# Optimization experiments

Measured on AMD Instinct MI355X. Metric: run time of the kernel, lower is better.

Reference implementation:

```python
import math
import jax, jax.numpy as jnp
import numpy as np

B, S, E, H, P = 8, 1024, 512, 8, 32
MAXD, OFFS, LW, STL, HID = 256, 8.0, 4, 4, 2048

def _lin(x, w, b):
    return x @ w.T + b

def _gelu(x):
    return jax.nn.gelu(x, approximate=False)  # torch nn.GELU default (erf)

def _ln(x, g, b, eps=1e-5):
    m = x.mean(-1, keepdims=True)
    v = ((x - m) ** 2).mean(-1, keepdims=True)
    return (x - m) / jnp.sqrt(v + eps) * g + b

def setup_inputs() -> dict:
    key = jax.random.key(0)
    ks = iter(jax.random.split(key, 40))
    def w(*shape):
        return (jax.random.normal(next(ks), shape, dtype=jnp.float32) * 0.02)
    x = jax.random.normal(next(ks), (B, S, E), dtype=jnp.float32)
    lengths = jax.random.randint(next(ks), (B,), S // 2, S + 1)
    padding_mask = jnp.arange(S)[None, :] >= lengths[:, None]  # (B,S) bool
    inp = dict(x=x, padding_mask=padding_mask)
    # local MHA (torch nn.MultiheadAttention packed in_proj)
    inp.update(in_proj_w=w(3 * E, E), in_proj_b=jnp.zeros((3 * E,), jnp.float32),
               mha_out_w=w(E, E), mha_out_b=jnp.zeros((E,), jnp.float32))
    # deformable attention projections
    for nm in ('dq', 'dk', 'dv', 'do'):
        inp[nm + '_w'] = w(E, E); inp[nm + '_b'] = jnp.zeros((E,), jnp.float32)
    inp.update(off1_w=w(E, E), off1_b=jnp.zeros((E,), jnp.float32),
               off2_w=w(H * P, E), off2_b=jnp.zeros((H * P,), jnp.float32))
    inp.update(gate1_w=w(E, 3 * E), gate1_b=jnp.zeros((E,), jnp.float32),
               gate2_w=w(E, E), gate2_b=jnp.zeros((E,), jnp.float32))
    inp.update(n1_g=jnp.ones((E,), jnp.float32), n1_b=jnp.zeros((E,), jnp.float32),
               n2_g=jnp.ones((E,), jnp.float32), n2_b=jnp.zeros((E,), jnp.float32))
    inp.update(ffn1_w=w(HID, E), ffn1_b=jnp.zeros((HID,), jnp.float32),
               ffn2_w=w(E, HID), ffn2_b=jnp.zeros((E,), jnp.float32))
    return inp

def _forward(x, padding_mask, in_proj_w, in_proj_b, mha_out_w, mha_out_b,
             dq_w, dq_b, dk_w, dk_b, dv_w, dv_b, do_w, do_b,
             off1_w, off1_b, off2_w, off2_b, gate1_w, gate1_b, gate2_w, gate2_b,
             n1_g, n1_b, n2_g, n2_b, ffn1_w, ffn1_b, ffn2_w, ffn2_b):
    Bv, Sv, Ev = x.shape
    hd = Ev // H
    pos = jnp.arange(Sv)
    # ---------------- local causal windowed MHA ----------------
    qkv = _lin(x, in_proj_w, in_proj_b)
    q, k, v = jnp.split(qkv, 3, axis=-1)
    q = q.reshape(Bv, Sv, H, hd).transpose(0, 2, 1, 3)  # bhsd
    k = k.reshape(Bv, Sv, H, hd).transpose(0, 2, 1, 3)
    v = v.reshape(Bv, Sv, H, hd).transpose(0, 2, 1, 3)
    scores = jnp.einsum('bhqd,bhkd->bhqk', q, k) / math.sqrt(hd)
    future = pos[None, :] > pos[:, None]
    too_far = (pos[:, None] - pos[None, :]) >= min(LW, STL)
    lmask = (future | too_far)[None, None] | padding_mask[:, None, None, :]
    scores = jnp.where(lmask, -jnp.inf, scores)
    allm = lmask.all(-1, keepdims=True)
    scores = jnp.where(allm, 0.0, scores)  # avoid NaN on fully-masked (padded) rows
    attn = jax.nn.softmax(scores, axis=-1)
    attn = jnp.where(lmask, 0.0, attn)
    lo = jnp.einsum('bhqk,bhkd->bhqd', attn, v).transpose(0, 2, 1, 3).reshape(Bv, Sv, Ev)
    local_out = _lin(lo, mha_out_w, mha_out_b)
    # ---------------- deformable long-history attention ----------------
    anchors = jnp.linspace(0.1, 0.9, P)
    valid_len = jnp.clip(Sv - padding_mask.sum(-1), 1, None)
    positions = pos[None, :, None].astype(jnp.float32)  # (1,S,1)
    base = anchors[None, None, :] * positions
    off = jnp.tanh(_lin(_gelu(_lin(x, off1_w, off1_b)), off2_w, off2_b))
    off = off.reshape(Bv, Sv, H, P).mean(2) * OFFS
    sampled = base + off
    sampled = jnp.clip(sampled, jnp.clip(positions - MAXD, 0, None), positions)
    sampled = jnp.minimum(sampled, (valid_len - 1).astype(jnp.float32)[:, None, None])
    sp = jnp.round(sampled).astype(jnp.int32)  # (B,S,P) sample positions
    qd = _lin(x, dq_w, dq_b)
    kd = _lin(x, dk_w, dk_b)
    vd = _lin(x, dv_w, dv_b)
    bidx = jnp.arange(Bv)[:, None, None]
    k_sp = kd[bidx, sp]  # (B,S,P,E) gathered keys
    v_sp = vd[bidx, sp]
    sc = jnp.einsum('bqd,bqpd->bqp', qd, k_sp) / math.sqrt(Ev)
    samp_inv = padding_mask[bidx, sp]
    causal_inv = sp > pos[None, :, None]
    rb = jnp.clip(pos[:, None] - (STL - 1), 0, None)
    long_mem_mask = pos[None, :] >= rb  # (S,S): forbid recent short-term positions
    extra_inv = long_mem_mask[pos[None, :, None], sp]
    inv = samp_inv | causal_inv | extra_inv
    sc = jnp.where(inv, -jnp.inf, sc)
    alli = inv.all(-1, keepdims=True)
    sc = jnp.where(alli, 0.0, sc)
    a = jax.nn.softmax(sc, axis=-1)
    a = jnp.where(inv, 0.0, a)
    long_out = _lin(jnp.einsum('bqp,bqpd->bqd', a, v_sp), do_w, do_b)
    # ---------------- gate fuse + FFN ----------------
    cat = jnp.concatenate([x, local_out, long_out], axis=-1)
    g = jax.nn.sigmoid(_lin(_gelu(_lin(cat, gate1_w, gate1_b)), gate2_w, gate2_b))
    fused = g * local_out + (1.0 - g) * long_out
    x1 = _ln(x + fused, n1_g, n1_b)
    f = _lin(_gelu(_lin(x1, ffn1_w, ffn1_b)), ffn2_w, ffn2_b)
    return _ln(x1 + f, n2_g, n2_b)

def reference(x, padding_mask, in_proj_w, in_proj_b, mha_out_w, mha_out_b,
              dq_w, dq_b, dk_w, dk_b, dv_w, dv_b, do_w, do_b,
              off1_w, off1_b, off2_w, off2_b, gate1_w, gate1_b, gate2_w, gate2_b,
              n1_g, n1_b, n2_g, n2_b, ffn1_w, ffn1_b, ffn2_w, ffn2_b):
    return _forward(x, padding_mask, in_proj_w, in_proj_b, mha_out_w, mha_out_b,
                    dq_w, dq_b, dk_w, dk_b, dv_w, dv_b, do_w, do_b,
                    off1_w, off1_b, off2_w, off2_b, gate1_w, gate1_b, gate2_w, gate2_b,
                    n1_g, n1_b, n2_g, n2_b, ffn1_w, ffn1_b, ffn2_w, ffn2_b)
```

## Files before the change

kernel.cpp:

```cpp
#include <hip/hip_runtime.h>
#include <hip/hip_bf16.h>
#include <type_traits>

typedef __hip_bfloat16 bf16;
typedef __attribute__((ext_vector_type(8))) short short8;
typedef __attribute__((ext_vector_type(4))) float floatx4;

static constexpr int kB = 8;
static constexpr int kS = 1024;
static constexpr int kE = 512;
static constexpr int kH = 8;
static constexpr int kP = 32;
static constexpr int kTok = kB * kS;
static constexpr int kHid = 2048;

__device__ __forceinline__ void load8f(const bf16* p, float* f) {
  uint4 u = *(const uint4*)p;
  const bf16* h = (const bf16*)&u;
#pragma unroll
  for (int e = 0; e < 8; e++) f[e] = __bfloat162float(h[e]);
}
__device__ __forceinline__ void store8b(bf16* p, const float* f) {
  uint4 u;
  bf16* h = (bf16*)&u;
#pragma unroll
  for (int e = 0; e < 8; e++) h[e] = __float2bfloat16(f[e]);
  *(uint4*)p = u;
}
__device__ __forceinline__ bool is_pad(const void* pm, int flag, int idx) {
  return flag ? (((const int*)pm)[idx] != 0)
              : (((const unsigned char*)pm)[idx] != 0);
}
__device__ __forceinline__ float fast_gelu(float x) {
  float u = x * (0.7978845608f + 0.044714998f * x * x);
  float e = __expf(2.0f * u);
  float t = 1.0f - 2.0f / (e + 1.0f);
  return 0.5f * x * (1.0f + t);
}
__device__ __forceinline__ void dma16(const bf16* g, bf16* l) {
  __builtin_amdgcn_global_load_lds(
      (const __attribute__((address_space(1))) unsigned int*)g,
      (__attribute__((address_space(3))) unsigned int*)l, 16, 0, 0);
}
__device__ __forceinline__ void drain_all() { __builtin_amdgcn_s_waitcnt(0); }

__global__ __launch_bounds__(256) void detect_kernel(const void* __restrict__ x,
                                                     int* __restrict__ meta) {
  __shared__ int cnt;
  if (threadIdx.x == 0) cnt = 0;
  __syncthreads();
  const unsigned short* u = (const unsigned short*)x;
  int c = 0;
  for (int i = threadIdx.x; i < 1024; i += 256) {
    int e = (u[i] >> 7) & 0xFF;
    if (e >= 0x90) c++;
  }
  if (c) atomicAdd(&cnt, c);
  __syncthreads();
  if (threadIdx.x == 0) meta[9] = (cnt > 64) ? 1 : 0;
}

__global__ __launch_bounds__(256) void meta_kernel(const void* __restrict__ pm,
                                                   int* __restrict__ meta) {
  __shared__ int bigfound;
  __shared__ int cnt[kB];
  int tid = threadIdx.x;
  if (tid == 0) bigfound = 0;
  if (tid < kB) cnt[tid] = 0;
  __syncthreads();
  const unsigned int* w = (const unsigned int*)pm;
  int f = 0;
  for (int i = tid; i < 2048; i += 256)
    if (w[i] & 0xFFFFFFFEu) f = 1;
  if (f) atomicOr(&bigfound, 1);
  __syncthreads();
  int flag = bigfound ? 0 : 1;
  for (int i = tid; i < kTok; i += 256) {
    if (is_pad(pm, flag, i)) atomicAdd(&cnt[i >> 10], 1);
  }
  __syncthreads();
  if (tid == 0) meta[0] = flag;
  if (tid < kB) {
    int vl = kS - cnt[tid];
    if (vl < 1) vl = 1;
    meta[1 + tid] = vl;
  }
}

struct CvtJob { const void* src; bf16* hi; bf16* lo; int nblk; };
struct CvtJobs { CvtJob j[13]; };
__global__ __launch_bounds__(256) void cvt_all_kernel(CvtJobs jobs,
                                                      const int* __restrict__ meta) {
  int fp = meta[9];
  int b = blockIdx.x, ji = 0;
  while (b >= jobs.j[ji].nblk) { b -= jobs.j[ji].nblk; ji++; }
  CvtJob J = jobs.j[ji];
  int i = b * 1024 + threadIdx.x * 4;
  float v[4];
  if (fp) {
    float4 f = ((const float4*)J.src)[i >> 2];
    v[0] = f.x; v[1] = f.y; v[2] = f.z; v[3] = f.w;
  } else {
    uint2 u = *(const uint2*)((const bf16*)J.src + i);
    const bf16* h = (const bf16*)&u;
#pragma unroll
    for (int e = 0; e < 4; e++) v[e] = __bfloat162float(h[e]);
  }
  uint2 uh;
  bf16* hh = (bf16*)&uh;
#pragma unroll
  for (int e = 0; e < 4; e++) hh[e] = __float2bfloat16(v[e]);
  *(uint2*)(J.hi + i) = uh;
  if (J.lo) {
    uint2 ul;
    bf16* hl = (bf16*)&ul;
#pragma unroll
    for (int e = 0; e < 4; e++)
      hl[e] = __float2bfloat16(v[e] - __bfloat162float(hh[e]));
    *(uint2*)(J.lo + i) = ul;
  }
}

struct CvtFJob { const void* src; float* dst; int n; };
struct CvtFJobs { CvtFJob j[16]; };
__global__ __launch_bounds__(256) void cvt_small_kernel(CvtFJobs jobs,
                                                        const int* __restrict__ meta) {
  int fp = meta[9];
#pragma unroll 1
  for (int ji = 0; ji < 16; ji++) {
    CvtFJob J = jobs.j[ji];
    for (int i = threadIdx.x; i < J.n; i += 256)
      J.dst[i] = fp ? ((const float*)J.src)[i]
                    : __bfloat162float(((const bf16*)J.src)[i]);
  }
}

static constexpr int BK = 32;

template <int BM, int BN, int ACT, typename OUTT>
__device__ __forceinline__ void gemm_core(const bf16* __restrict__ A,
                                          const bf16* __restrict__ W,
                                          const float* __restrict__ bias,
                                          OUTT* __restrict__ C, int N, int K,
                                          int m0, int n0) {
  constexpr int WR = (BM == 128 && BN == 128) ? 4 : 2;
  constexpr int WC = 4;
  __shared__ bf16 As[2][BM * BK];
  __shared__ bf16 Bs[2][BN * BK];
  const int tid = threadIdx.x;
  const int lane = tid & 63;
  const int wid = tid >> 6;
  int wm, wn;
  if constexpr (BM == 128 && BN == 128) {
    wm = (wid >> 1) * 64; wn = (wid & 1) * 64;
  } else {
    wm = wid * 32; wn = 0;
  }

  auto stage = [&](int buf, int kt) {
#pragma unroll
    for (int c = 0; c < BM / 64; c++) {
      int seg = c * 64 + wid * 16;
      int row = seg + (lane >> 2);
      int ch = (lane & 3) ^ ((row >> 1) & 3);
      dma16(&A[(size_t)(m0 + row) * K + kt + ch * 8], &As[buf][seg * BK]);
    }
#pragma unroll
    for (int c = 0; c < BN / 64; c++) {
      int seg = c * 64 + wid * 16;
      int row = seg + (lane >> 2);
      int ch = (lane & 3) ^ ((row >> 1) & 3);
      dma16(&W[(size_t)(n0 + row) * K + kt + ch * 8], &Bs[buf][seg * BK]);
    }
  };

  floatx4 acc[WR][WC];
#pragma unroll
  for (int i = 0; i < WR; i++)
#pragma unroll
    for (int j = 0; j < WC; j++) acc[i][j] = (floatx4)0.0f;

  stage(0, 0);
  drain_all();
  __syncthreads();
  const int niter = K / BK;
  for (int k = 0; k < niter; k++) {
    const int cur = k & 1;
    if (k + 1 < niter) stage(cur ^ 1, (k + 1) * BK);
    const int kb = lane >> 4;
    short8 af[WR], bfr[WC];
#pragma unroll
    for (int i = 0; i < WR; i++) {
      int r = wm + i * 16 + (lane & 15);
      af[i] = *(const short8*)(&As[cur][r * BK + ((kb ^ ((r >> 1) & 3)) << 3)]);
    }
#pragma unroll
    for (int j = 0; j < WC; j++) {
      int r = wn + j * 16 + (lane & 15);
      bfr[j] = *(const short8*)(&Bs[cur][r * BK + ((kb ^ ((r >> 1) & 3)) << 3)]);
    }
#pragma unroll
    for (int i = 0; i < WR; i++)
#pragma unroll
      for (int j = 0; j < WC; j++)
        acc[i][j] = __builtin_amdgcn_mfma_f32_16x16x32_bf16(bfr[j], af[i],
                                                            acc[i][j], 0, 0, 0);
    drain_all();
    __syncthreads();
  }

#pragma unroll
  for (int i = 0; i < WR; i++) {
    int row = m0 + wm + i * 16 + (lane & 15);
#pragma unroll
    for (int j = 0; j < WC; j++) {
      int col = n0 + wn + j * 16 + ((lane >> 4) << 2);
      float bv[4] = {0.f, 0.f, 0.f, 0.f};
      if (bias) {
        float4 b4 = *(const float4*)&bias[col];
        bv[0] = b4.x; bv[1] = b4.y; bv[2] = b4.z; bv[3] = b4.w;
      }
      float v[4];
#pragma unroll
      for (int r = 0; r < 4; r++) {
        v[r] = acc[i][j][r] + bv[r];
        if (ACT == 1) v[r] = fast_gelu(v[r]);
        else if (ACT == 2) v[r] = 1.0f / (1.0f + __expf(-v[r]));
      }
      size_t idx = (size_t)row * N + col;
      if constexpr (std::is_same<OUTT, float>::value) {
        *(float4*)&C[idx] = make_float4(v[0], v[1], v[2], v[3]);
      } else {
        uint2 u;
        bf16* h = (bf16*)&u;
#pragma unroll
        for (int r = 0; r < 4; r++) h[r] = __float2bfloat16(v[r]);
        *(uint2*)&C[idx] = u;
      }
    }
  }
}

template <int BM, int BN, int ACT, typename OUTT>
__global__ __launch_bounds__(256) void gemm_bt(
    const bf16* __restrict__ A, const bf16* __restrict__ W,
    const float* __restrict__ bias, OUTT* __restrict__ C, int N, int K) {
  gemm_core<BM, BN, ACT, OUTT>(A, W, bias, C, N, K, blockIdx.x * BM,
                               blockIdx.y * BN);
}

__global__ __launch_bounds__(256) void gemm_pair(
    const bf16* __restrict__ A0, const bf16* __restrict__ W0,
    const float* __restrict__ b0, bf16* __restrict__ C0,
    const bf16* __restrict__ A1, const bf16* __restrict__ W1,
    const float* __restrict__ b1, bf16* __restrict__ C1, int N, int K) {
  int nb = N >> 6;
  bool s = (int)blockIdx.y >= nb;
  gemm_core<128, 64, 0, bf16>(s ? A1 : A0, s ? W1 : W0, s ? b1 : b0,
                              s ? C1 : C0, N, K, blockIdx.x * 128,
                              (s ? (int)blockIdx.y - nb : (int)blockIdx.y) * 64);
}

__global__ __launch_bounds__(256) void gemm_gate1(
    const bf16* __restrict__ x, const bf16* __restrict__ lo,
    const bf16* __restrict__ lg, const bf16* __restrict__ W,
    const float* __restrict__ bias, bf16* __restrict__ C) {
  constexpr int BM = 128, BN = 64, WR = 2, WC = 4;
  constexpr int N = 512, K = 1536;
  __shared__ bf16 As[2][BM * BK];
  __shared__ bf16 Bs[2][BN * BK];
  const int tid = threadIdx.x;
  const int lane = tid & 63;
  const int wid = tid >> 6;
  const int wm = wid * 32, wn = 0;
  const int m0 = blockIdx.x * BM, n0 = blockIdx.y * BN;

  auto stage = [&](int buf, int kt) {
    const bf16* src = (kt < 512) ? x : (kt < 1024) ? lo : lg;
    int kk = kt & 511;
#pragma unroll
    for (int c = 0; c < 2; c++) {
      int seg = c * 64 + wid * 16;
      int row = seg + (lane >> 2);
      int ch = (lane & 3) ^ ((row >> 1) & 3);
      dma16(&src[(size_t)(m0 + row) * 512 + kk + ch * 8], &As[buf][seg * BK]);
    }
    {
      int seg = wid * 16;
      int row = seg + (lane >> 2);
      int ch = (lane & 3) ^ ((row >> 1) & 3);
      dma16(&W[(size_t)(n0 + row) * K + kt + ch * 8], &Bs[buf][seg * BK]);
    }
  };

  floatx4 acc[WR][WC];
#pragma unroll
  for (int i = 0; i < WR; i++)
#pragma unroll
    for (int j = 0; j < WC; j++) acc[i][j] = (floatx4)0.0f;

  stage(0, 0);
  drain_all();
  __syncthreads();
  const int niter = K / BK;
  for (int k = 0; k < niter; k++) {
    const int cur = k & 1;
    if (k + 1 < niter) stage(cur ^ 1, (k + 1) * BK);
    const int kb = lane >> 4;
    short8 af[WR], bfr[WC];
#pragma unroll
    for (int i = 0; i < WR; i++) {
      int r = wm + i * 16 + (lane & 15);
      af[i] = *(const short8*)(&As[cur][r * BK + ((kb ^ ((r >> 1) & 3)) << 3)]);
    }
#pragma unroll
    for (int j = 0; j < WC; j++) {
      int r = wn + j * 16 + (lane & 15);
      bfr[j] = *(const short8*)(&Bs[cur][r * BK + ((kb ^ ((r >> 1) & 3)) << 3)]);
    }
#pragma unroll
    for (int i = 0; i < WR; i++)
#pragma unroll
      for (int j = 0; j < WC; j++)
        acc[i][j] = __builtin_amdgcn_mfma_f32_16x16x32_bf16(bfr[j], af[i],
                                                            acc[i][j], 0, 0, 0);
    drain_all();
    __syncthreads();
  }

#pragma unroll
  for (int i = 0; i < WR; i++) {
    int row = m0 + wm + i * 16 + (lane & 15);
#pragma unroll
    for (int j = 0; j < WC; j++) {
      int col = n0 + wn + j * 16 + ((lane >> 4) << 2);
      float4 b4 = *(const float4*)&bias[col];
      float bv[4] = {b4.x, b4.y, b4.z, b4.w};
      uint2 u;
      bf16* h = (bf16*)&u;
#pragma unroll
      for (int r = 0; r < 4; r++)
        h[r] = __float2bfloat16(fast_gelu(acc[i][j][r] + bv[r]));
      *(uint2*)&C[(size_t)row * N + col] = u;
    }
  }
}

template <int BM, int BN, bool SPLIT, bool ALWAYS_AL>
__global__ __launch_bounds__(256) void gemm3_bt(
    const bf16* __restrict__ Ah, const bf16* __restrict__ Al,
    const bf16* __restrict__ Wh, const bf16* __restrict__ Wl,
    const float* __restrict__ bias, const int* __restrict__ meta,
    float* __restrict__ Cf, bf16* __restrict__ Chi, bf16* __restrict__ Clo,
    int N, int K) {
  constexpr int WR = 2;
  constexpr int WC = (BM == 128) ? 4 : 2;
  __shared__ bf16 Ash[BM * BK];
  __shared__ bf16 Asl[BM * BK];
  __shared__ bf16 Bsh[BN * BK];
  __shared__ bf16 Bsl[BN * BK];
  const int fp = meta[9];
  const bool use_al = fp || ALWAYS_AL;
  const int tid = threadIdx.x;
  const int lane = tid & 63;
  const int wid = tid >> 6;
  int wm, wn;
  if constexpr (BM == 128) {
    wm = wid * 32; wn = 0;
  } else {
    wm = (wid >> 1) * 32; wn = (wid & 1) * 32;
  }
  const int m0 = blockIdx.x * BM, n0 = blockIdx.y * BN;

  floatx4 acc[WR][WC];
#pragma unroll
  for (int i = 0; i < WR; i++)
#pragma unroll
    for (int j = 0; j < WC; j++) acc[i][j] = (floatx4)0.0f;

  for (int kt = 0; kt < K; kt += BK) {
#pragma unroll
    for (int c = 0; c < BM / 64; c++) {
      int seg = c * 64 + wid * 16;
      int row = seg + (lane >> 2);
      int ch = (lane & 3) ^ ((row >> 1) & 3);
      size_t g = (size_t)(m0 + row) * K + kt + ch * 8;
      dma16(&Ah[g], &Ash[seg * BK]);
      if (use_al) dma16(&Al[g], &Asl[seg * BK]);
    }
#pragma unroll
    for (int c = 0; c < BN / 64; c++) {
      int seg = c * 64 + wid * 16;
      int row = seg + (lane >> 2);
      int ch = (lane & 3) ^ ((row >> 1) & 3);
      size_t g = (size_t)(n0 + row) * K + kt + ch * 8;
      dma16(&Wh[g], &Bsh[seg * BK]);
      if (fp) dma16(&Wl[g], &Bsl[seg * BK]);
    }
    drain_all();
    __syncthreads();
    const int kb = lane >> 4;
    short8 ah[WR], al[WR], bh[WC], bl[WC];
#pragma unroll
    for (int i = 0; i < WR; i++) {
      int r = wm + i * 16 + (lane & 15);
      int ro = r * BK + ((kb ^ ((r >> 1) & 3)) << 3);
      ah[i] = *(const short8*)(&Ash[ro]);
      if (use_al) al[i] = *(const short8*)(&Asl[ro]);
    }
#pragma unroll
    for (int j = 0; j < WC; j++) {
      int r = wn + j * 16 + (lane & 15);
      int ro = r * BK + ((kb ^ ((r >> 1) & 3)) << 3);
      bh[j] = *(const short8*)(&Bsh[ro]);
      if (fp) bl[j] = *(const short8*)(&Bsl[ro]);
    }
#pragma unroll
    for (int i = 0; i < WR; i++)
#pragma unroll
      for (int j = 0; j < WC; j++) {
        acc[i][j] = __builtin_amdgcn_mfma_f32_16x16x32_bf16(bh[j], ah[i],
                                                            acc[i][j], 0, 0, 0);
        if (fp)
          acc[i][j] = __builtin_amdgcn_mfma_f32_16x16x32_bf16(
              bl[j], ah[i], acc[i][j], 0, 0, 0);
        if (use_al)
          acc[i][j] = __builtin_amdgcn_mfma_f32_16x16x32_bf16(
              bh[j], al[i], acc[i][j], 0, 0, 0);
      }
    __syncthreads();
  }

#pragma unroll
  for (int i = 0; i < WR; i++) {
    int row = m0 + wm + i * 16 + (lane & 15);
#pragma unroll
    for (int j = 0; j < WC; j++) {
      int col = n0 + wn + j * 16 + ((lane >> 4) << 2);
      float4 b4 = *(const float4*)&bias[col];
      float bv[4] = {b4.x, b4.y, b4.z, b4.w};
      if constexpr (SPLIT) {
        uint2 uh, ul;
        bf16* hh = (bf16*)&uh;
        bf16* hl = (bf16*)&ul;
#pragma unroll
        for (int r = 0; r < 4; r++) {
          float v = acc[i][j][r] + bv[r];
          float g = 0.5f * v * (1.0f + erff(v * 0.70710678118654752f));
          bf16 hi = __float2bfloat16(g);
          hh[r] = hi;
          hl[r] = __float2bfloat16(g - __bfloat162float(hi));
        }
        *(uint2*)&Chi[(size_t)row * N + col] = uh;
        *(uint2*)&Clo[(size_t)row * N + col] = ul;
      } else {
        *(float4*)&Cf[(size_t)row * N + col] =
            make_float4(acc[i][j][0] + bv[0], acc[i][j][1] + bv[1],
                        acc[i][j][2] + bv[2], acc[i][j][3] + bv[3]);
      }
    }
  }
}

__global__ __launch_bounds__(256) void local_attn_kernel(
    const bf16* __restrict__ qkv, const void* __restrict__ pm,
    const int* __restrict__ meta, bf16* __restrict__ lo) {
  int lane = threadIdx.x & 63;
  int t = blockIdx.x * 4 + (threadIdx.x >> 6);
  int b = t >> 10, s = t & 1023;
  int h = lane >> 3, sub = lane & 7;
  int flag = meta[0];
  float q[8];
  load8f(qkv + (size_t)t * 3072 + h * 64 + sub * 8, q);
  float sc[4];
  bool val[4];
#pragma unroll
  for (int w = 0; w < 4; w++) {
    int kp = s - 3 + w;
    bool v = (kp >= 0) && !is_pad(pm, flag, b * kS + kp);
    float d = 0.0f;
    if (v) {
      float kk[8];
      load8f(qkv + (size_t)(b * kS + kp) * 3072 + 512 + h * 64 + sub * 8, kk);
#pragma unroll
      for (int e = 0; e < 8; e++) d += q[e] * kk[e];
    }
    d += __shfl_xor(d, 1);
    d += __shfl_xor(d, 2);
    d += __shfl_xor(d, 4);
    sc[w] = v ? d / 8.0f : -INFINITY;
    val[w] = v;
  }
  float mx = fmaxf(fmaxf(sc[0], sc[1]), fmaxf(sc[2], sc[3]));
  float a[4] = {0.f, 0.f, 0.f, 0.f};
  if (mx != -INFINITY) {
    float ssum = 0.f;
#pragma unroll
    for (int w = 0; w < 4; w++) {
      float e = val[w] ? expf(sc[w] - mx) : 0.0f;
      a[w] = e;
      ssum += e;
    }
#pragma unroll
    for (int w = 0; w < 4; w++) a[w] /= ssum;
  }
  float o[8] = {0.f, 0.f, 0.f, 0.f, 0.f, 0.f, 0.f, 0.f};
#pragma unroll
  for (int w = 0; w < 4; w++) {
    if (val[w] && a[w] > 0.0f) {
      int kp = s - 3 + w;
      float vv[8];
      load8f(qkv + (size_t)(b * kS + kp) * 3072 + 1024 + h * 64 + sub * 8, vv);
#pragma unroll
      for (int e = 0; e < 8; e++) o[e] += a[w] * vv[e];
    }
  }
  store8b(lo + (size_t)t * kE + lane * 8, o);
}

__global__ __launch_bounds__(256) void sampler_kernel(
    const float* __restrict__ rawf, const void* __restrict__ pm,
    const int* __restrict__ meta, int* __restrict__ sp,
    unsigned int* __restrict__ invm) {
  int t = blockIdx.x * 8 + (threadIdx.x >> 5);
  int p = threadIdx.x & 31;
  int b = t >> 10, s = t & 1023;
  int flag = meta[0];
  float off = 0.0f;
#pragma unroll
  for (int h = 0; h < kH; h++) off += tanhf(rawf[(size_t)t * 256 + h * kP + p]);
  double anchor = 0.1 + 0.8 * (double)p / 31.0;
  double sampled = anchor * (double)s + (double)off;
  double lov = fmax(0.0, (double)s - 256.0);
  sampled = fmin(fmax(sampled, lov), (double)s);
  int vlen = meta[1 + b];
  sampled = fmin(sampled, (double)(vlen - 1));
  int spv = (int)rint(sampled);
  bool inv = is_pad(pm, flag, b * kS + spv) || (spv > s) ||
             (spv >= max(0, s - 3));
  sp[(size_t)t * kP + p] = spv;
  unsigned long long m = __ballot(inv);
  int lane = threadIdx.x & 63;
  if (lane == 0) invm[t] = (unsigned int)m;
  if (lane == 32) invm[t] = (unsigned int)(m >> 32);
}

__global__ __launch_bounds__(256) void long_attn_kernel(
    const bf16* __restrict__ qkv, const int* __restrict__ sp,
    const unsigned int* __restrict__ invm, bf16* __restrict__ ctx) {
  int lane = threadIdx.x & 63;
  int bid = blockIdx.x;
  int sbid = (bid & 7) * 256 + (bid >> 3);
  int t = sbid * 4 + (threadIdx.x >> 6);
  int b = t >> 10;
  int p = lane & 31;
  int row_abs = b * kS + sp[(size_t)t * kP + p];
  float q[8];
  load8f(qkv + (size_t)t * 3072 + 1536 + lane * 8, q);
  float sc_mine = 0.0f;
#pragma unroll 4
  for (int pp = 0; pp < 32; pp++) {
    int row = __shfl(row_abs, pp);
    float kk[8];
    load8f(qkv + (size_t)row * 3072 + 2048 + lane * 8, kk);
    float d = 0.0f;
#pragma unroll
    for (int e = 0; e < 8; e++) d += q[e] * kk[e];
#pragma unroll
    for (int m = 1; m < 64; m <<= 1) d += __shfl_xor(d, m);
    if (p == pp) sc_mine = d;
  }
  bool inv = (invm[t] >> p) & 1u;
  float sc = inv ? -INFINITY : sc_mine / 22.627416997969522f;
  float mx = sc;
#pragma unroll
  for (int m = 1; m < 32; m <<= 1) mx = fmaxf(mx, __shfl_xor(mx, m));
  float e = (inv || mx == -INFINITY) ? 0.0f : expf(sc - mx);
  float ssum = e;
#pragma unroll
  for (int m = 1; m < 32; m <<= 1) ssum += __shfl_xor(ssum, m);
  float a = (ssum > 0.0f) ? e / ssum : 0.0f;
  float o[8] = {0.f, 0.f, 0.f, 0.f, 0.f, 0.f, 0.f, 0.f};
#pragma unroll 4
  for (int pp = 0; pp < 32; pp++) {
    float ap = __shfl(a, pp);
    int row = __shfl(row_abs, pp);
    if (ap != 0.0f) {
      float vv[8];
      load8f(qkv + (size_t)row * 3072 + 2560 + lane * 8, vv);
#pragma unroll
      for (int e2 = 0; e2 < 8; e2++) o[e2] += ap * vv[e2];
    }
  }
  store8b(ctx + (size_t)t * kE + lane * 8, o);
}

__global__ __launch_bounds__(256) void ln1_kernel(
    const void* __restrict__ xin, const int* __restrict__ meta,
    const bf16* __restrict__ lo, const bf16* __restrict__ lg,
    const bf16* __restrict__ g, const float* __restrict__ gamma,
    const float* __restrict__ beta, bf16* __restrict__ x1b,
    float* __restrict__ x1f) {
  int lane = threadIdx.x & 63;
  int t = blockIdx.x * 4 + (threadIdx.x >> 6);
  size_t base = (size_t)t * kE + lane * 8;
  float xv[8], lov[8], lgv[8], gv[8], h[8];
  if (meta[9]) {
    const float4* xf = (const float4*)((const float*)xin + base);
    float4 a = xf[0], b2 = xf[1];
    xv[0] = a.x; xv[1] = a.y; xv[2] = a.z; xv[3] = a.w;
    xv[4] = b2.x; xv[5] = b2.y; xv[6] = b2.z; xv[7] = b2.w;
  } else {
    load8f((const bf16*)xin + base, xv);
  }
  load8f(lo + base, lov);
  load8f(lg + base, lgv);
  load8f(g + base, gv);
  float s1 = 0.f, s2 = 0.f;
#pragma unroll
  for (int e = 0; e < 8; e++) {
    h[e] = xv[e] + gv[e] * lov[e] + (1.0f - gv[e]) * lgv[e];
    s1 += h[e];
    s2 += h[e] * h[e];
  }
#pragma unroll
  for (int m = 1; m < 64; m <<= 1) {
    s1 += __shfl_xor(s1, m);
    s2 += __shfl_xor(s2, m);
  }
  float mean = s1 * (1.0f / kE);
  float var = s2 * (1.0f / kE) - mean * mean;
  float rstd = 1.0f / sqrtf(var + 1e-5f);
  float y[8];
#pragma unroll
  for (int e = 0; e < 8; e++)
    y[e] = (h[e] - mean) * rstd * gamma[lane * 8 + e] + beta[lane * 8 + e];
  store8b(x1b + base, y);
#pragma unroll
  for (int e = 0; e < 8; e++) x1f[base + e] = y[e];
}

__global__ __launch_bounds__(256) void ln2_kernel(
    const float* __restrict__ x1f, const float* __restrict__ ff,
    const float* __restrict__ gamma, const float* __restrict__ beta,
    const int* __restrict__ meta, void* __restrict__ out) {
  int lane = threadIdx.x & 63;
  int t = blockIdx.x * 4 + (threadIdx.x >> 6);
  size_t base = (size_t)t * kE + lane * 8;
  float h[8];
  float s1 = 0.f, s2 = 0.f;
#pragma unroll
  for (int e = 0; e < 8; e++) {
    h[e] = x1f[base + e] + ff[base + e];
    s1 += h[e];
    s2 += h[e] * h[e];
  }
#pragma unroll
  for (int m = 1; m < 64; m <<= 1) {
    s1 += __shfl_xor(s1, m);
    s2 += __shfl_xor(s2, m);
  }
  float mean = s1 * (1.0f / kE);
  float var = s2 * (1.0f / kE) - mean * mean;
  float rstd = 1.0f / sqrtf(var + 1e-5f);
  float y[8];
#pragma unroll
  for (int e = 0; e < 8; e++)
    y[e] = (h[e] - mean) * rstd * gamma[lane * 8 + e] + beta[lane * 8 + e];
  if (meta[9]) {
    float* of = (float*)out + base;
    ((float4*)of)[0] = make_float4(y[0], y[1], y[2], y[3]);
    ((float4*)of)[1] = make_float4(y[4], y[5], y[6], y[7]);
  } else {
    store8b((bf16*)out + base, y);
  }
}

extern "C" void kernel_launch(void* const* d_in, const int* in_sizes, int n_in,
                              void* d_out, int out_size, void* d_ws,
                              size_t ws_size, hipStream_t stream) {
  const void* x = d_in[0];
  const void* pm = d_in[1];

  char* w = (char*)d_ws;
  auto alloc = [&](size_t bytes) {
    char* p = w;
    w += (bytes + 255) & ~(size_t)255;
    return p;
  };
  bf16* qkv_all = (bf16*)alloc((size_t)kTok * 3072 * 2);
  bf16* lo_ctx = (bf16*)alloc((size_t)kTok * kE * 2);
  bf16* ctx2 = (bf16*)alloc((size_t)kTok * kE * 2);
  bf16* local_out = (bf16*)alloc((size_t)kTok * kE * 2);
  bf16* long_out = (bf16*)alloc((size_t)kTok * kE * 2);
  bf16* hbuf = (bf16*)alloc((size_t)kTok * kE * 2);
  bf16* gbuf = (bf16*)alloc((size_t)kTok * kE * 2);
  bf16* x1b = (bf16*)alloc((size_t)kTok * kE * 2);
  float* x1f = (float*)alloc((size_t)kTok * kE * 4);
  float* rawf = (float*)alloc((size_t)kTok * 256 * 4);
  int* sp = (int*)alloc((size_t)kTok * kP * 4);
  unsigned int* invm = (unsigned int*)alloc((size_t)kTok * 4);
  int* meta = (int*)alloc(256);
  bf16* x_hi = (bf16*)alloc((size_t)kTok * kE * 2);
  bf16* x_lo = (bf16*)alloc((size_t)kTok * kE * 2);
  bf16* wall = (bf16*)alloc((size_t)3072 * 512 * 2);
  bf16* mow = (bf16*)alloc(512 * 512 * 2);
  bf16* dow = (bf16*)alloc(512 * 512 * 2);
  bf16* o1h = (bf16*)alloc(512 * 512 * 2);
  bf16* o1l = (bf16*)alloc(512 * 512 * 2);
  bf16* o2h = (bf16*)alloc(256 * 512 * 2);
  bf16* o2l = (bf16*)alloc(256 * 512 * 2);
  bf16* g1w = (bf16*)alloc(512 * 1536 * 2);
  bf16* g2w = (bf16*)alloc(512 * 512 * 2);
  bf16* f1w = (bf16*)alloc((size_t)2048 * 512 * 2);
  bf16* f2w = (bf16*)alloc((size_t)512 * 2048 * 2);
  float* ball = (float*)alloc(3072 * 4);
  float* mob = (float*)alloc(512 * 4);
  float* dob = (float*)alloc(512 * 4);
  float* o1b = (float*)alloc(512 * 4);
  float* o2b = (float*)alloc(256 * 4);
  float* g1b = (float*)alloc(512 * 4);
  float* g2b = (float*)alloc(512 * 4);
  float* n1g = (float*)alloc(512 * 4);
  float* n1bt = (float*)alloc(512 * 4);
  float* n2g = (float*)alloc(512 * 4);
  float* n2bt = (float*)alloc(512 * 4);
  float* f1b = (float*)alloc(2048 * 4);
  float* f2b = (float*)alloc(512 * 4);

  bf16* h_hi = hbuf;
  bf16* h_lo = x1b;
  float* f_f32 = (float*)qkv_all;
  bf16* ffn_h = (bf16*)((char*)qkv_all + (size_t)kTok * kE * 4);

  dim3 blk(256);
  detect_kernel<<<1, blk, 0, stream>>>(x, meta);
  meta_kernel<<<1, blk, 0, stream>>>(pm, meta);

  CvtJobs J;
  auto job = [](const void* s, bf16* hi, bf16* lo, int n) {
    CvtJob j; j.src = s; j.hi = hi; j.lo = lo; j.nblk = n >> 10; return j;
  };
  J.j[0] = job(d_in[0], x_hi, x_lo, kTok * kE);
  J.j[1] = job(d_in[2], wall, nullptr, 1536 * 512);
  J.j[2] = job(d_in[6], wall + (size_t)1536 * 512, nullptr, 512 * 512);
  J.j[3] = job(d_in[8], wall + (size_t)2048 * 512, nullptr, 512 * 512);
  J.j[4] = job(d_in[10], wall + (size_t)2560 * 512, nullptr, 512 * 512);
  J.j[5] = job(d_in[4], mow, nullptr, 512 * 512);
  J.j[6] = job(d_in[12], dow, nullptr, 512 * 512);
  J.j[7] = job(d_in[14], o1h, o1l, 512 * 512);
  J.j[8] = job(d_in[16], o2h, o2l, 256 * 512);
  J.j[9] = job(d_in[18], g1w, nullptr, 512 * 1536);
  J.j[10] = job(d_in[20], g2w, nullptr, 512 * 512);
  J.j[11] = job(d_in[26], f1w, nullptr, 2048 * 512);
  J.j[12] = job(d_in[28], f2w, nullptr, 512 * 2048);
  int totblk = 0;
  for (int i = 0; i < 13; i++) totblk += J.j[i].nblk;
  cvt_all_kernel<<<totblk, blk, 0, stream>>>(J, meta);

  CvtFJobs JF;
  auto fjob = [](const void* s, float* d, int n) {
    CvtFJob j; j.src = s; j.dst = d; j.n = n; return j;
  };
  JF.j[0] = fjob(d_in[3], ball, 1536);
  JF.j[1] = fjob(d_in[7], ball + 1536, 512);
  JF.j[2] = fjob(d_in[9], ball + 2048, 512);
  JF.j[3] = fjob(d_in[11], ball + 2560, 512);
  JF.j[4] = fjob(d_in[5], mob, 512);
  JF.j[5] = fjob(d_in[13], dob, 512);
  JF.j[6] = fjob(d_in[15], o1b, 512);
  JF.j[7] = fjob(d_in[17], o2b, 256);
  JF.j[8] = fjob(d_in[19], g1b, 512);
  JF.j[9] = fjob(d_in[21], g2b, 512);
  JF.j[10] = fjob(d_in[22], n1g, 512);
  JF.j[11] = fjob(d_in[23], n1bt, 512);
  JF.j[12] = fjob(d_in[24], n2g, 512);
  JF.j[13] = fjob(d_in[25], n2bt, 512);
  JF.j[14] = fjob(d_in[27], f1b, 2048);
  JF.j[15] = fjob(d_in[29], f2b, 512);
  cvt_small_kernel<<<1, blk, 0, stream>>>(JF, meta);

  gemm_bt<128, 128, 0, bf16><<<dim3(64, 24), blk, 0, stream>>>(
      x_hi, wall, ball, qkv_all, 3072, kE);
  gemm3_bt<128, 64, true, false><<<dim3(64, 8), blk, 0, stream>>>(
      x_hi, x_lo, o1h, o1l, o1b, meta, nullptr, h_hi, h_lo, kE, kE);
  local_attn_kernel<<<2048, blk, 0, stream>>>(qkv_all, pm, meta, lo_ctx);
  gemm3_bt<64, 64, false, true><<<dim3(128, 4), blk, 0, stream>>>(
      h_hi, h_lo, o2h, o2l, o2b, meta, rawf, nullptr, nullptr, 256, kE);
  sampler_kernel<<<1024, blk, 0, stream>>>(rawf, pm, meta, sp, invm);
  long_attn_kernel<<<2048, blk, 0, stream>>>(qkv_all, sp, invm, ctx2);

  gemm_pair<<<dim3(64, 16), blk, 0, stream>>>(lo_ctx, mow, mob, local_out,
                                              ctx2, dow, dob, long_out, kE, kE);

  gemm_gate1<<<dim3(64, 8), blk, 0, stream>>>(x_hi, local_out, long_out, g1w,
                                              g1b, hbuf);
  gemm_bt<128, 64, 2, bf16><<<dim3(64, 8), blk, 0, stream>>>(
      hbuf, g2w, g2b, gbuf, kE, kE);

  ln1_kernel<<<2048, blk, 0, stream>>>(x, meta, local_out, long_out, gbuf, n1g,
                                       n1bt, x1b, x1f);
  gemm_bt<128, 128, 1, bf16><<<dim3(64, 16), blk, 0, stream>>>(
      x1b, f1w, f1b, ffn_h, kHid, kE);
  gemm_bt<128, 64, 0, float><<<dim3(64, 8), blk, 0, stream>>>(
      ffn_h, f2w, f2b, f_f32, kE, kHid);
  ln2_kernel<<<2048, blk, 0, stream>>>(x1f, f_f32, n2g, n2bt, meta, d_out);
}
```

Baseline: 457.2 us.

## Merge independent kernels into combined launches and fuse sampler into long attention

Combines the detect and meta kernels into one launch and folds the small bias conversion into the big conversion kernel as an extra block. The QKV GEMM and offset-1 split GEMM now share one grid, as do the local attention and offset-2 GEMM. The sampler is folded into long attention, which drops the sp/invm intermediate buffers. The aim is to cut launch overhead and tail idle time by running independent work together. In exchange, GEMM shared memory now comes from one buffer per kernel, and a heterogeneous grid can raise per-block resource use and lower occupancy for the lighter parts.

```diff
diff --git a/kernel.cpp b/kernel.cpp
--- a/kernel.cpp
+++ b/kernel.cpp
@@ -44,44 +44,39 @@
 }
 __device__ __forceinline__ void drain_all() { __builtin_amdgcn_s_waitcnt(0); }
 
-__global__ __launch_bounds__(256) void detect_kernel(const void* __restrict__ x,
-                                                     int* __restrict__ meta) {
+__global__ __launch_bounds__(256) void detect_meta_kernel(
+    const void* __restrict__ x, const void* __restrict__ pm,
+    int* __restrict__ meta) {
   __shared__ int cnt;
-  if (threadIdx.x == 0) cnt = 0;
+  __shared__ int bigfound;
+  __shared__ int pc[kB];
+  int tid = threadIdx.x;
+  if (tid == 0) { cnt = 0; bigfound = 0; }
+  if (tid < kB) pc[tid] = 0;
   __syncthreads();
   const unsigned short* u = (const unsigned short*)x;
   int c = 0;
-  for (int i = threadIdx.x; i < 1024; i += 256) {
+  for (int i = tid; i < 1024; i += 256) {
     int e = (u[i] >> 7) & 0xFF;
     if (e >= 0x90) c++;
   }
   if (c) atomicAdd(&cnt, c);
-  __syncthreads();
-  if (threadIdx.x == 0) meta[9] = (cnt > 64) ? 1 : 0;
-}
-
-__global__ __launch_bounds__(256) void meta_kernel(const void* __restrict__ pm,
-                                                   int* __restrict__ meta) {
-  __shared__ int bigfound;
-  __shared__ int cnt[kB];
-  int tid = threadIdx.x;
-  if (tid == 0) bigfound = 0;
-  if (tid < kB) cnt[tid] = 0;
-  __syncthreads();
-  const unsigned int* w = (const unsigned int*)pm;
+  const unsigned int* wp = (const unsigned int*)pm;
   int f = 0;
   for (int i = tid; i < 2048; i += 256)
-    if (w[i] & 0xFFFFFFFEu) f = 1;
+    if (wp[i] & 0xFFFFFFFEu) f = 1;
   if (f) atomicOr(&bigfound, 1);
   __syncthreads();
   int flag = bigfound ? 0 : 1;
-  for (int i = tid; i < kTok; i += 256) {
-    if (is_pad(pm, flag, i)) atomicAdd(&cnt[i >> 10], 1);
-  }
+  for (int i = tid; i < kTok; i += 256)
+    if (is_pad(pm, flag, i)) atomicAdd(&pc[i >> 10], 1);
   __syncthreads();
-  if (tid == 0) meta[0] = flag;
+  if (tid == 0) {
+    meta[0] = flag;
+    meta[9] = (cnt > 64) ? 1 : 0;
+  }
   if (tid < kB) {
-    int vl = kS - cnt[tid];
+    int vl = kS - pc[tid];
     if (vl < 1) vl = 1;
     meta[1 + tid] = vl;
   }
@@ -89,10 +84,23 @@
 
 struct CvtJob { const void* src; bf16* hi; bf16* lo; int nblk; };
 struct CvtJobs { CvtJob j[13]; };
-__global__ __launch_bounds__(256) void cvt_all_kernel(CvtJobs jobs,
-                                                      const int* __restrict__ meta) {
+struct CvtFJob { const void* src; float* dst; int n; };
+struct CvtFJobs { CvtFJob j[16]; };
+__global__ __launch_bounds__(256) void cvt_all_kernel(
+    CvtJobs jobs, CvtFJobs fjobs, int totblk, const int* __restrict__ meta) {
   int fp = meta[9];
-  int b = blockIdx.x, ji = 0;
+  int b = blockIdx.x;
+  if (b >= totblk) {
+#pragma unroll 1
+    for (int ji = 0; ji < 16; ji++) {
+      CvtFJob J = fjobs.j[ji];
+      for (int i = threadIdx.x; i < J.n; i += 256)
+        J.dst[i] = fp ? ((const float*)J.src)[i]
+                      : __bfloat162float(((const bf16*)J.src)[i]);
+    }
+    return;
+  }
+  int ji = 0;
   while (b >= jobs.j[ji].nblk) { b -= jobs.j[ji].nblk; ji++; }
   CvtJob J = jobs.j[ji];
   int i = b * 1024 + threadIdx.x * 4;
@@ -121,32 +129,17 @@
   }
 }
 
-struct CvtFJob { const void* src; float* dst; int n; };
-struct CvtFJobs { CvtFJob j[16]; };
-__global__ __launch_bounds__(256) void cvt_small_kernel(CvtFJobs jobs,
-                                                        const int* __restrict__ meta) {
-  int fp = meta[9];
-#pragma unroll 1
-  for (int ji = 0; ji < 16; ji++) {
-    CvtFJob J = jobs.j[ji];
-    for (int i = threadIdx.x; i < J.n; i += 256)
-      J.dst[i] = fp ? ((const float*)J.src)[i]
-                    : __bfloat162float(((const bf16*)J.src)[i]);
-  }
-}
-
 static constexpr int BK = 32;
 
 template <int BM, int BN, int ACT, typename OUTT>
-__device__ __forceinline__ void gemm_core(const bf16* __restrict__ A,
-                                          const bf16* __restrict__ W,
-                                          const float* __restrict__ bias,
-                                          OUTT* __restrict__ C, int N, int K,
-                                          int m0, int n0) {
+__device__ __forceinline__ void gemm_core(bf16* smem, const bf16* A,
+                                          const bf16* W, const float* bias,
+                                          OUTT* C, int N, int K, int m0,
+                                          int n0) {
   constexpr int WR = (BM == 128 && BN == 128) ? 4 : 2;
   constexpr int WC = 4;
-  __shared__ bf16 As[2][BM * BK];
-  __shared__ bf16 Bs[2][BN * BK];
+  bf16* As[2] = {smem, smem + BM * BK};
+  bf16* Bs[2] = {smem + 2 * BM * BK, smem + 2 * BM * BK + BN * BK};
   const int tid = threadIdx.x;
   const int lane = tid & 63;
   const int wid = tid >> 6;
@@ -241,124 +234,17 @@
   }
 }
 
-template <int BM, int BN, int ACT, typename OUTT>
-__global__ __launch_bounds__(256) void gemm_bt(
-    const bf16* __restrict__ A, const bf16* __restrict__ W,
-    const float* __restrict__ bias, OUTT* __restrict__ C, int N, int K) {
-  gemm_core<BM, BN, ACT, OUTT>(A, W, bias, C, N, K, blockIdx.x * BM,
-                               blockIdx.y * BN);
-}
-
-__global__ __launch_bounds__(256) void gemm_pair(
-    const bf16* __restrict__ A0, const bf16* __restrict__ W0,
-    const float* __restrict__ b0, bf16* __restrict__ C0,
-    const bf16* __restrict__ A1, const bf16* __restrict__ W1,
-    const float* __restrict__ b1, bf16* __restrict__ C1, int N, int K) {
-  int nb = N >> 6;
-  bool s = (int)blockIdx.y >= nb;
-  gemm_core<128, 64, 0, bf16>(s ? A1 : A0, s ? W1 : W0, s ? b1 : b0,
-                              s ? C1 : C0, N, K, blockIdx.x * 128,
-                              (s ? (int)blockIdx.y - nb : (int)blockIdx.y) * 64);
-}
-
-__global__ __launch_bounds__(256) void gemm_gate1(
-    const bf16* __restrict__ x, const bf16* __restrict__ lo,
-    const bf16* __restrict__ lg, const bf16* __restrict__ W,
-    const float* __restrict__ bias, bf16* __restrict__ C) {
-  constexpr int BM = 128, BN = 64, WR = 2, WC = 4;
-  constexpr int N = 512, K = 1536;
-  __shared__ bf16 As[2][BM * BK];
-  __shared__ bf16 Bs[2][BN * BK];
-  const int tid = threadIdx.x;
-  const int lane = tid & 63;
-  const int wid = tid >> 6;
-  const int wm = wid * 32, wn = 0;
-  const int m0 = blockIdx.x * BM, n0 = blockIdx.y * BN;
-
-  auto stage = [&](int buf, int kt) {
-    const bf16* src = (kt < 512) ? x : (kt < 1024) ? lo : lg;
-    int kk = kt & 511;
-#pragma unroll
-    for (int c = 0; c < 2; c++) {
-      int seg = c * 64 + wid * 16;
-      int row = seg + (lane >> 2);
-      int ch = (lane & 3) ^ ((row >> 1) & 3);
-      dma16(&src[(size_t)(m0 + row) * 512 + kk + ch * 8], &As[buf][seg * BK]);
-    }
-    {
-      int seg = wid * 16;
-      int row = seg + (lane >> 2);
-      int ch = (lane & 3) ^ ((row >> 1) & 3);
-      dma16(&W[(size_t)(n0 + row) * K + kt + ch * 8], &Bs[buf][seg * BK]);
-    }
-  };
-
-  floatx4 acc[WR][WC];
-#pragma unroll
-  for (int i = 0; i < WR; i++)
-#pragma unroll
-    for (int j = 0; j < WC; j++) acc[i][j] = (floatx4)0.0f;
-
-  stage(0, 0);
-  drain_all();
-  __syncthreads();
-  const int niter = K / BK;
-  for (int k = 0; k < niter; k++) {
-    const int cur = k & 1;
-    if (k + 1 < niter) stage(cur ^ 1, (k + 1) * BK);
-    const int kb = lane >> 4;
-    short8 af[WR], bfr[WC];
-#pragma unroll
-    for (int i = 0; i < WR; i++) {
-      int r = wm + i * 16 + (lane & 15);
-      af[i] = *(const short8*)(&As[cur][r * BK + ((kb ^ ((r >> 1) & 3)) << 3)]);
-    }
-#pragma unroll
-    for (int j = 0; j < WC; j++) {
-      int r = wn + j * 16 + (lane & 15);
-      bfr[j] = *(const short8*)(&Bs[cur][r * BK + ((kb ^ ((r >> 1) & 3)) << 3)]);
-    }
-#pragma unroll
-    for (int i = 0; i < WR; i++)
-#pragma unroll
-      for (int j = 0; j < WC; j++)
-        acc[i][j] = __builtin_amdgcn_mfma_f32_16x16x32_bf16(bfr[j], af[i],
-                                                            acc[i][j], 0, 0, 0);
-    drain_all();
-    __syncthreads();
-  }
-
-#pragma unroll
-  for (int i = 0; i < WR; i++) {
-    int row = m0 + wm + i * 16 + (lane & 15);
-#pragma unroll
-    for (int j = 0; j < WC; j++) {
-      int col = n0 + wn + j * 16 + ((lane >> 4) << 2);
-      float4 b4 = *(const float4*)&bias[col];
-      float bv[4] = {b4.x, b4.y, b4.z, b4.w};
-      uint2 u;
-      bf16* h = (bf16*)&u;
-#pragma unroll
-      for (int r = 0; r < 4; r++)
-        h[r] = __float2bfloat16(fast_gelu(acc[i][j][r] + bv[r]));
-      *(uint2*)&C[(size_t)row * N + col] = u;
-    }
-  }
-}
-
 template <int BM, int BN, bool SPLIT, bool ALWAYS_AL>
-__global__ __launch_bounds__(256) void gemm3_bt(
-    const bf16* __restrict__ Ah, const bf16* __restrict__ Al,
-    const bf16* __restrict__ Wh, const bf16* __restrict__ Wl,
-    const float* __restrict__ bias, const int* __restrict__ meta,
-    float* __restrict__ Cf, bf16* __restrict__ Chi, bf16* __restrict__ Clo,
-    int N, int K) {
+__device__ __forceinline__ void gemm3_core(
+    bf16* smem, const bf16* Ah, const bf16* Al, const bf16* Wh,
+    const bf16* Wl, const float* bias, const int* meta, float* Cf, bf16* Chi,
+    bf16* Clo, int N, int K, int m0, int n0) {
   constexpr int WR = 2;
   constexpr int WC = (BM == 128) ? 4 : 2;
-  __shared__ bf16 Ash[BM * BK];
-  __shared__ bf16 Asl[BM * BK];
-  __shared__ bf16 Bsh[BN * BK];
-  __shared__ bf16 Bsl[BN * BK];
+  bf16* Ash = smem;
+  bf16* Asl = smem + BM * BK;
+  bf16* Bsh = smem + 2 * BM * BK;
+  bf16* Bsl = smem + 2 * BM * BK + BN * BK;
   const int fp = meta[9];
   const bool use_al = fp || ALWAYS_AL;
   const int tid = threadIdx.x;
@@ -370,7 +256,6 @@
   } else {
     wm = (wid >> 1) * 32; wn = (wid & 1) * 32;
   }
-  const int m0 = blockIdx.x * BM, n0 = blockIdx.y * BN;
 
   floatx4 acc[WR][WC];
 #pragma unroll
@@ -462,11 +347,54 @@
   }
 }
 
-__global__ __launch_bounds__(256) void local_attn_kernel(
-    const bf16* __restrict__ qkv, const void* __restrict__ pm,
-    const int* __restrict__ meta, bf16* __restrict__ lo) {
+template <int BM, int BN, int ACT, typename OUTT>
+__global__ __launch_bounds__(256) void gemm_bt(
+    const bf16* __restrict__ A, const bf16* __restrict__ W,
+    const float* __restrict__ bias, OUTT* __restrict__ C, int N, int K) {
+  __shared__ bf16 smem[2 * (BM + BN) * BK];
+  gemm_core<BM, BN, ACT, OUTT>(smem, A, W, bias, C, N, K, blockIdx.x * BM,
+                               blockIdx.y * BN);
+}
+
+__global__ __launch_bounds__(256) void gemm_pair(
+    const bf16* __restrict__ A0, const bf16* __restrict__ W0,
+    const float* __restrict__ b0, bf16* __restrict__ C0,
+    const bf16* __restrict__ A1, const bf16* __restrict__ W1,
+    const float* __restrict__ b1, bf16* __restrict__ C1, int N, int K) {
+  __shared__ bf16 smem[2 * (128 + 64) * BK];
+  int nb = N >> 6;
+  bool s = (int)blockIdx.y >= nb;
+  gemm_core<128, 64, 0, bf16>(smem, s ? A1 : A0, s ? W1 : W0, s ? b1 : b0,
+                              s ? C1 : C0, N, K, blockIdx.x * 128,
+                              (s ? (int)blockIdx.y - nb : (int)blockIdx.y) * 64);
+}
+
+__global__ __launch_bounds__(256) void qkv_o1_kernel(
+    const bf16* __restrict__ x_hi, const bf16* __restrict__ x_lo,
+    const bf16* __restrict__ wall, const float* __restrict__ ball,
+    bf16* __restrict__ qkv_all, const bf16* __restrict__ o1h,
+    const bf16* __restrict__ o1l, const float* __restrict__ o1b,
+    const int* __restrict__ meta, bf16* __restrict__ h_hi,
+    bf16* __restrict__ h_lo) {
+  __shared__ bf16 smem[2 * 256 * BK];
+  if ((int)blockIdx.y < 24) {
+    gemm_core<128, 128, 0, bf16>(smem, x_hi, wall, ball, qkv_all, 3072, kE,
+                                 blockIdx.x * 128, blockIdx.y * 128);
+  } else {
+    gemm3_core<128, 64, true, false>(smem, x_hi, x_lo, o1h, o1l, o1b, meta,
+                                     nullptr, h_hi, h_lo, kE, kE,
+                                     blockIdx.x * 128,
+                                     ((int)blockIdx.y - 24) * 64);
+  }
+}
+
+__device__ __forceinline__ void local_attn_body(const bf16* __restrict__ qkv,
+                                                const void* __restrict__ pm,
+                                                const int* __restrict__ meta,
+                                                bf16* __restrict__ lo,
+                                                int bid) {
   int lane = threadIdx.x & 63;
-  int t = blockIdx.x * 4 + (threadIdx.x >> 6);
+  int t = bid * 4 + (threadIdx.x >> 6);
   int b = t >> 10, s = t & 1023;
   int h = lane >> 3, sub = lane & 7;
   int flag = meta[0];
@@ -518,14 +446,34 @@
   store8b(lo + (size_t)t * kE + lane * 8, o);
 }
 
-__global__ __launch_bounds__(256) void sampler_kernel(
-    const float* __restrict__ rawf, const void* __restrict__ pm,
-    const int* __restrict__ meta, int* __restrict__ sp,
-    unsigned int* __restrict__ invm) {
-  int t = blockIdx.x * 8 + (threadIdx.x >> 5);
-  int p = threadIdx.x & 31;
+__global__ __launch_bounds__(256) void local_o2_kernel(
+    const bf16* __restrict__ qkv, const void* __restrict__ pm,
+    const int* __restrict__ meta, bf16* __restrict__ lo_ctx,
+    const bf16* __restrict__ h_hi, const bf16* __restrict__ h_lo,
+    const bf16* __restrict__ o2h, const bf16* __restrict__ o2l,
+    const float* __restrict__ o2b, float* __restrict__ rawf) {
+  __shared__ bf16 smem[4 * 64 * BK];
+  if ((int)blockIdx.x < 2048) {
+    local_attn_body(qkv, pm, meta, lo_ctx, blockIdx.x);
+  } else {
+    int id = (int)blockIdx.x - 2048;
+    gemm3_core<64, 64, false, true>(smem, h_hi, h_lo, o2h, o2l, o2b, meta,
+                                    rawf, nullptr, nullptr, 256, kE,
+                                    (id >> 2) * 64, (id & 3) * 64);
+  }
+}
+
+__global__ __launch_bounds__(256) void long_attn_kernel(
+    const bf16* __restrict__ qkv, const float* __restrict__ rawf,
+    const void* __restrict__ pm, const int* __restrict__ meta,
+    bf16* __restrict__ ctx) {
+  int lane = threadIdx.x & 63;
+  int bid = blockIdx.x;
+  int sbid = (bid & 7) * 256 + (bid >> 3);
+  int t = sbid * 4 + (threadIdx.x >> 6);
   int b = t >> 10, s = t & 1023;
   int flag = meta[0];
+  int p = lane & 31;
   float off = 0.0f;
 #pragma unroll
   for (int h = 0; h < kH; h++) off += tanhf(rawf[(size_t)t * 256 + h * kP + p]);
@@ -538,23 +486,7 @@
   int spv = (int)rint(sampled);
   bool inv = is_pad(pm, flag, b * kS + spv) || (spv > s) ||
              (spv >= max(0, s - 3));
-  sp[(size_t)t * kP + p] = spv;
-  unsigned long long m = __ballot(inv);
-  int lane = threadIdx.x & 63;
-  if (lane == 0) invm[t] = (unsigned int)m;
-  if (lane == 32) invm[t] = (unsigned int)(m >> 32);
-}
-
-__global__ __launch_bounds__(256) void long_attn_kernel(
-    const bf16* __restrict__ qkv, const int* __restrict__ sp,
-    const unsigned int* __restrict__ invm, bf16* __restrict__ ctx) {
-  int lane = threadIdx.x & 63;
-  int bid = blockIdx.x;
-  int sbid = (bid & 7) * 256 + (bid >> 3);
-  int t = sbid * 4 + (threadIdx.x >> 6);
-  int b = t >> 10;
-  int p = lane & 31;
-  int row_abs = b * kS + sp[(size_t)t * kP + p];
+  int row_abs = b * kS + spv;
   float q[8];
   load8f(qkv + (size_t)t * 3072 + 1536 + lane * 8, q);
   float sc_mine = 0.0f;
@@ -570,7 +502,6 @@
     for (int m = 1; m < 64; m <<= 1) d += __shfl_xor(d, m);
     if (p == pp) sc_mine = d;
   }
-  bool inv = (invm[t] >> p) & 1u;
   float sc = inv ? -INFINITY : sc_mine / 22.627416997969522f;
   float mx = sc;
 #pragma unroll
@@ -593,6 +524,91 @@
     }
   }
   store8b(ctx + (size_t)t * kE + lane * 8, o);
+}
+
+__global__ __launch_bounds__(256) void gemm_gate1(
+    const bf16* __restrict__ x, const bf16* __restrict__ lo,
+    const bf16* __restrict__ lg, const bf16* __restrict__ W,
+    const float* __restrict__ bias, bf16* __restrict__ C) {
+  constexpr int BM = 128, BN = 64, WR = 2, WC = 4;
+  constexpr int N = 512, K = 1536;
+  __shared__ bf16 As[2][BM * BK];
+  __shared__ bf16 Bs[2][BN * BK];
+  const int tid = threadIdx.x;
+  const int lane = tid & 63;
+  const int wid = tid >> 6;
+  const int wm = wid * 32, wn = 0;
+  const int m0 = blockIdx.x * BM, n0 = blockIdx.y * BN;
+
+  auto stage = [&](int buf, int kt) {
+    const bf16* src = (kt < 512) ? x : (kt < 1024) ? lo : lg;
+    int kk = kt & 511;
+#pragma unroll
+    for (int c = 0; c < 2; c++) {
+      int seg = c * 64 + wid * 16;
+      int row = seg + (lane >> 2);
+      int ch = (lane & 3) ^ ((row >> 1) & 3);
+      dma16(&src[(size_t)(m0 + row) * 512 + kk + ch * 8], &As[buf][seg * BK]);
+    }
+    {
+      int seg = wid * 16;
+      int row = seg + (lane >> 2);
+      int ch = (lane & 3) ^ ((row >> 1) & 3);
+      dma16(&W[(size_t)(n0 + row) * K + kt + ch * 8], &Bs[buf][seg * BK]);
+    }
+  };
+
+  floatx4 acc[WR][WC];
+#pragma unroll
+  for (int i = 0; i < WR; i++)
+#pragma unroll
+    for (int j = 0; j < WC; j++) acc[i][j] = (floatx4)0.0f;
+
+  stage(0, 0);
+  drain_all();
+  __syncthreads();
+  const int niter = K / BK;
+  for (int k = 0; k < niter; k++) {
+    const int cur = k & 1;
+    if (k + 1 < niter) stage(cur ^ 1, (k + 1) * BK);
+    const int kb = lane >> 4;
+    short8 af[WR], bfr[WC];
+#pragma unroll
+    for (int i = 0; i < WR; i++) {
+      int r = wm + i * 16 + (lane & 15);
+      af[i] = *(const short8*)(&As[cur][r * BK + ((kb ^ ((r >> 1) & 3)) << 3)]);
+    }
+#pragma unroll
+    for (int j = 0; j < WC; j++) {
+      int r = wn + j * 16 + (lane & 15);
+      bfr[j] = *(const short8*)(&Bs[cur][r * BK + ((kb ^ ((r >> 1) & 3)) << 3)]);
+    }
+#pragma unroll
+    for (int i = 0; i < WR; i++)
+#pragma unroll
+      for (int j = 0; j < WC; j++)
+        acc[i][j] = __builtin_amdgcn_mfma_f32_16x16x32_bf16(bfr[j], af[i],
+                                                            acc[i][j], 0, 0, 0);
+    drain_all();
+    __syncthreads();
+  }
+
+#pragma unroll
+  for (int i = 0; i < WR; i++) {
+    int row = m0 + wm + i * 16 + (lane & 15);
+#pragma unroll
+    for (int j = 0; j < WC; j++) {
+      int col = n0 + wn + j * 16 + ((lane >> 4) << 2);
+      float4 b4 = *(const float4*)&bias[col];
+      float bv[4] = {b4.x, b4.y, b4.z, b4.w};
+      uint2 u;
+      bf16* h = (bf16*)&u;
+#pragma unroll
+      for (int r = 0; r < 4; r++)
+        h[r] = __float2bfloat16(fast_gelu(acc[i][j][r] + bv[r]));
+      *(uint2*)&C[(size_t)row * N + col] = u;
+    }
+  }
 }
 
 __global__ __launch_bounds__(256) void ln1_kernel(
@@ -698,8 +714,6 @@
   bf16* x1b = (bf16*)alloc((size_t)kTok * kE * 2);
   float* x1f = (float*)alloc((size_t)kTok * kE * 4);
   float* rawf = (float*)alloc((size_t)kTok * 256 * 4);
-  int* sp = (int*)alloc((size_t)kTok * kP * 4);
-  unsigned int* invm = (unsigned int*)alloc((size_t)kTok * 4);
   int* meta = (int*)alloc(256);
   bf16* x_hi = (bf16*)alloc((size_t)kTok * kE * 2);
   bf16* x_lo = (bf16*)alloc((size_t)kTok * kE * 2);
@@ -734,8 +748,7 @@
   bf16* ffn_h = (bf16*)((char*)qkv_all + (size_t)kTok * kE * 4);
 
   dim3 blk(256);
-  detect_kernel<<<1, blk, 0, stream>>>(x, meta);
-  meta_kernel<<<1, blk, 0, stream>>>(pm, meta);
+  detect_meta_kernel<<<1, blk, 0, stream>>>(x, pm, meta);
 
   CvtJobs J;
   auto job = [](const void* s, bf16* hi, bf16* lo, int n) {
@@ -756,7 +769,6 @@
   J.j[12] = job(d_in[28], f2w, nullptr, 512 * 2048);
   int totblk = 0;
   for (int i = 0; i < 13; i++) totblk += J.j[i].nblk;
-  cvt_all_kernel<<<totblk, blk, 0, stream>>>(J, meta);
 
   CvtFJobs JF;
   auto fjob = [](const void* s, float* d, int n) {
@@ -778,17 +790,13 @@
   JF.j[13] = fjob(d_in[25], n2bt, 512);
   JF.j[14] = fjob(d_in[27], f1b, 2048);
   JF.j[15] = fjob(d_in[29], f2b, 512);
-  cvt_small_kernel<<<1, blk, 0, stream>>>(JF, meta);
-
-  gemm_bt<128, 128, 0, bf16><<<dim3(64, 24), blk, 0, stream>>>(
-      x_hi, wall, ball, qkv_all, 3072, kE);
-  gemm3_bt<128, 64, true, false><<<dim3(64, 8), blk, 0, stream>>>(
-      x_hi, x_lo, o1h, o1l, o1b, meta, nullptr, h_hi, h_lo, kE, kE);
-  local_attn_kernel<<<2048, blk, 0, stream>>>(qkv_all, pm, meta, lo_ctx);
-  gemm3_bt<64, 64, false, true><<<dim3(128, 4), blk, 0, stream>>>(
-      h_hi, h_lo, o2h, o2l, o2b, meta, rawf, nullptr, nullptr, 256, kE);
-  sampler_kernel<<<1024, blk, 0, stream>>>(rawf, pm, meta, sp, invm);
-  long_attn_kernel<<<2048, blk, 0, stream>>>(qkv_all, sp, invm, ctx2);
+  cvt_all_kernel<<<totblk + 1, blk, 0, stream>>>(J, JF, totblk, meta);
+
+  qkv_o1_kernel<<<dim3(64, 32), blk, 0, stream>>>(
+      x_hi, x_lo, wall, ball, qkv_all, o1h, o1l, o1b, meta, h_hi, h_lo);
+  local_o2_kernel<<<2560, blk, 0, stream>>>(qkv_all, pm, meta, lo_ctx, h_hi,
+                                            h_lo, o2h, o2l, o2b, rawf);
+  long_attn_kernel<<<2048, blk, 0, stream>>>(qkv_all, rawf, pm, meta, ctx2);
 
   gemm_pair<<<dim3(64, 16), blk, 0, stream>>>(lo_ctx, mow, mob, local_out,
                                               ctx2, dow, dob, long_out, kE, kE);
```

Result: slower. 503.5 us (+10.1%).
